# Optimization experiments

Hardware: AMD Instinct MI355X
Metric: run time of the kernel (lower is better)

The kernel has to match this reference:

```python
import jax, jax.numpy as jnp
import numpy as np

# dims matching init_kwargs / input_specs
B, C, H = 8, 256, 48          # input (B, C, H, H)
GRID = 3                       # sqrt(num_memory)
NUM_MEM = GRID * GRID          # 9
WS = H // GRID                 # window_size = 16
S = 128                        # num_slots
D = WS * WS * C                # slot_dim = 65536
K = 5                          # gumbel top-k threshold (shrink_thres, int)
EPS = 1e-12


def setup_inputs() -> dict:
    key = jax.random.key(0)
    k1, k2, k3 = jax.random.split(key, 3)
    stdv = 1.0 / np.sqrt(D)
    x = jax.random.normal(k1, (B, C, H, H), dtype=jnp.float32)
    mem1 = jax.random.uniform(k2, (NUM_MEM, S, D), jnp.float32, -stdv, stdv)
    mem2 = jax.random.uniform(k3, (NUM_MEM, S, D), jnp.float32, -stdv, stdv)
    return {"x": x, "mem1": mem1, "mem2": mem2}


def _window_partition(x):
    # (B, C, H, W) -> (B, NUM_MEM, WS*WS*C); per-window layout is (ws, ws, C) row-major,
    # matching torch unfold -> view(B,C,ws^2,L) -> permute(0,3,2,1).
    b = x.shape[0]
    x = jnp.transpose(x, (0, 2, 3, 1))                        # (B, H, W, C)
    x = x.reshape(b, GRID, WS, GRID, WS, C)
    x = jnp.transpose(x, (0, 1, 3, 2, 4, 5))                  # (B, gh, gw, ws, ws, C)
    return x.reshape(b, NUM_MEM, WS * WS * C)


def _window_reverse(w):
    # (B, NUM_MEM, WS*WS*C) -> (B, C, H, W); exact inverse of _window_partition.
    b = w.shape[0]
    w = w.reshape(b, GRID, GRID, WS, WS, C)
    w = jnp.transpose(w, (0, 1, 3, 2, 4, 5)).reshape(b, H, H, C)
    return jnp.transpose(w, (0, 3, 1, 2))


def _hard_shrink_relu(y, lambd):
    d = y - lambd
    return jax.nn.relu(d) * y / (jnp.abs(d) + EPS)


def _memory_read(q, mem):
    # q: (B, M, D) window queries; mem: (M, S, D) per-window memory matrices.
    att = jnp.einsum('bmd,msd->bms', q, mem)                  # (B, M, S)
    y = jax.nn.softmax(att, axis=-1)
    k = min(S - 1, K)
    thres = jax.lax.top_k(y, k)[0][..., -1:]                  # kth largest per row
    y_hard = _hard_shrink_relu(y, thres)
    y_hard = y_hard / jnp.maximum(jnp.sum(jnp.abs(y_hard), axis=-1, keepdims=True), EPS)
    y_hard = jax.lax.stop_gradient(y_hard - y) + y            # straight-through
    return jnp.einsum('bms,msd->bmd', y_hard, mem)            # (B, M, D)


def reference(x, mem1, mem2):
    # CRU modeled as identity split: x1 = x2 = x (CRU source not provided).
    q = _window_partition(x)                                  # (B, 9, D)
    out1 = _window_reverse(_memory_read(q, mem1))
    out2 = _window_reverse(_memory_read(q, mem2))
    return out1 + out2                                        # eval mode: no bernoulli mask
```

## Files before the change

### kernel.cpp

```cpp
#include <hip/hip_runtime.h>
#include <hip/hip_bf16.h>
#include <cstdint>

#define Bn 8
#define Cn 256
#define Hn 48
#define NUM_MEM 9
#define WSZ 16
#define Sn 128
#define Dn 65536
#define KTOP 5
#define ND2 16

__global__ __launch_bounds__(256) void k_x2q(const float* __restrict__ x,
                                             float* __restrict__ q) {
    const int h = blockIdx.x;
    const int b = blockIdx.y;
    const int gh = h >> 4, i = h & 15;
    __shared__ float tile[Cn * Hn];
    const float* xp = x + (size_t)b * Cn * Hn * Hn + (size_t)h * Hn;
    for (int o = threadIdx.x; o < Cn * Hn; o += blockDim.x) {
        int c = o / Hn, w = o - c * Hn;
        tile[o] = xp[(size_t)c * Hn * Hn + w];
    }
    __syncthreads();
    for (int gw = 0; gw < 3; ++gw) {
        float* qp = q + (size_t)(b * NUM_MEM + gh * 3 + gw) * Dn + i * (WSZ * Cn);
        for (int l = threadIdx.x; l < WSZ * Cn; l += blockDim.x) {
            int j = l >> 8, c = l & 255;
            qp[l] = tile[c * Hn + gw * WSZ + j];
        }
    }
}

__global__ __launch_bounds__(256) void k_att3(const float* __restrict__ q,
                                              const float* __restrict__ mem1,
                                              const float* __restrict__ mem2,
                                              float* __restrict__ ap) {
    const int dseg = blockIdx.x;
    const int mw   = blockIdx.y;
    const int sgrp = blockIdx.z;
    const int e    = sgrp >> 3;
    const int lane = threadIdx.x & 63, wave = threadIdx.x >> 6;
    const int s0   = (sgrp & 7) * 16 + wave * 4;

    const float4* mem4 = (const float4*)(e ? mem2 : mem1);
    const float4* q4   = (const float4*)q;

    const int off0 = dseg * 1024 + lane;
    const float4* mr[4];
    const float4* qr[8];
#pragma unroll
    for (int r = 0; r < 4; ++r)
        mr[r] = mem4 + (size_t)(mw * Sn + s0 + r) * (Dn / 4) + off0;
#pragma unroll
    for (int b = 0; b < 8; ++b)
        qr[b] = q4 + (size_t)(b * NUM_MEM + mw) * (Dn / 4) + off0;

    float a[32];
#pragma unroll
    for (int i = 0; i < 32; ++i) a[i] = 0.f;

    float4 M[4], Q[8];
#pragma unroll
    for (int r = 0; r < 4; ++r) M[r] = mr[r][0];
#pragma unroll
    for (int b = 0; b < 8; ++b) Q[b] = qr[b][0];

    for (int step = 0; step < 16; ++step) {
        const int noff = (step < 15 ? step + 1 : step) * 64;
        float4 Mn[4], Qn[8];
#pragma unroll
        for (int r = 0; r < 4; ++r) Mn[r] = mr[r][noff];
#pragma unroll
        for (int b = 0; b < 8; ++b) Qn[b] = qr[b][noff];

#pragma unroll
        for (int r = 0; r < 4; ++r)
#pragma unroll
            for (int b = 0; b < 8; ++b) {
                a[r * 8 + b] += M[r].x * Q[b].x + M[r].y * Q[b].y
                              + M[r].z * Q[b].z + M[r].w * Q[b].w;
            }
#pragma unroll
        for (int r = 0; r < 4; ++r) M[r] = Mn[r];
#pragma unroll
        for (int b = 0; b < 8; ++b) Q[b] = Qn[b];
    }

#pragma unroll
    for (int k = 0; k < 5; ++k) {
        const int mk = 1 << k;
        const bool up = (lane & mk) != 0;
#pragma unroll
        for (int j = 0; j < (32 >> (k + 1)); ++j) {
            float lo = a[2 * j], hi = a[2 * j + 1];
            float mine = up ? hi : lo;
            float oth  = __shfl_xor(up ? lo : hi, mk, 64);
            a[j] = mine + oth;
        }
    }
    float rsum = a[0] + __shfl_xor(a[0], 32, 64);
    if (lane < 32) {
        const int b = lane & 7, r = (lane >> 3) & 3;
        const int s = s0 + r;
        ap[((size_t)dseg * 144 + (size_t)(e * 8 + b) * 9 + mw) * Sn + s] = rsum;
    }
}

__global__ __launch_bounds__(128) void k_smax(const float* __restrict__ ap,
                                              float* __restrict__ w) {
    const int row = blockIdx.x;
    const int t = threadIdx.x;
    __shared__ float sf[Sn];
    __shared__ unsigned long long sk[Sn];

    float v = 0.f;
#pragma unroll
    for (int nd = 0; nd < ND2; ++nd)
        v += ap[((size_t)nd * 144 + row) * Sn + t];

    sf[t] = v; __syncthreads();
    for (int s = 64; s > 0; s >>= 1) { if (t < s) sf[t] = fmaxf(sf[t], sf[t + s]); __syncthreads(); }
    float mx = sf[0]; __syncthreads();

    float e = expf(v - mx);
    sf[t] = e; __syncthreads();
    for (int s = 64; s > 0; s >>= 1) { if (t < s) sf[t] += sf[t + s]; __syncthreads(); }
    float sum = sf[0]; __syncthreads();
    float y = e / sum;

    bool alive = true;
    float thres = 0.f;
    unsigned int ybits = __float_as_uint(y);
    for (int it = 0; it < KTOP; ++it) {
        sk[t] = alive ? ((((unsigned long long)ybits) << 32) | (unsigned)t) : 0ull;
        __syncthreads();
        for (int s = 64; s > 0; s >>= 1) {
            if (t < s) { if (sk[t + s] > sk[t]) sk[t] = sk[t + s]; }
            __syncthreads();
        }
        unsigned long long kmax = sk[0];
        __syncthreads();
        if ((unsigned)(kmax & 0xffffffffull) == (unsigned)t) alive = false;
        thres = __uint_as_float((unsigned)(kmax >> 32));
    }

    float d   = y - thres;
    float num = fmaxf(d, 0.f) * y;
    float yh  = num / (fabsf(d) + 1e-12f);

    sf[t] = yh; __syncthreads();
    for (int s = 64; s > 0; s >>= 1) { if (t < s) sf[t] += sf[t + s]; __syncthreads(); }
    float l1 = sf[0];
    w[(size_t)row * Sn + t] = yh / fmaxf(l1, 1e-12f);
}

__global__ __launch_bounds__(256) void k_acc(const float* __restrict__ w,
                                             const float* __restrict__ mem1,
                                             const float* __restrict__ mem2,
                                             float* __restrict__ acc) {
    const int chunk = blockIdx.x;
    const int m     = blockIdx.y;
    const int b     = blockIdx.z;
    __shared__ int   nz[2];
    __shared__ int   idx[2][16];
    __shared__ float wv[2][16];
    if (threadIdx.x < 2) nz[threadIdx.x] = 0;
    __syncthreads();
    {
        int eidx = threadIdx.x >> 7;
        int s    = threadIdx.x & 127;
        float ww = w[((size_t)(eidx * Bn + b) * NUM_MEM + m) * Sn + s];
        if (ww != 0.f) {
            int p = atomicAdd(&nz[eidx], 1);
            if (p < 16) { idx[eidx][p] = s; wv[eidx][p] = ww; }
        }
    }
    __syncthreads();
    const int n1 = nz[0], n2 = nz[1];
    const size_t mbase = (size_t)m * Sn * Dn;
    const int dbase = chunk * 4096;
    for (int l = threadIdx.x * 4; l < 4096; l += 1024) {
        int d = dbase + l;
        float4 a = {0.f, 0.f, 0.f, 0.f};
        for (int j = 0; j < n1; ++j) {
            const float4 r = *(const float4*)(mem1 + mbase + (size_t)idx[0][j] * Dn + d);
            float ww = wv[0][j];
            a.x += ww * r.x; a.y += ww * r.y; a.z += ww * r.z; a.w += ww * r.w;
        }
        for (int j = 0; j < n2; ++j) {
            const float4 r = *(const float4*)(mem2 + mbase + (size_t)idx[1][j] * Dn + d);
            float ww = wv[1][j];
            a.x += ww * r.x; a.y += ww * r.y; a.z += ww * r.z; a.w += ww * r.w;
        }
        *(float4*)(acc + (size_t)(b * NUM_MEM + m) * Dn + d) = a;
    }
}

__global__ __launch_bounds__(256) void k_q2x(const float* __restrict__ acc,
                                             float* __restrict__ out) {
    const int h = blockIdx.x;
    const int b = blockIdx.y;
    const int gh = h >> 4, i = h & 15;
    __shared__ float tile[Cn * Hn];
    for (int gw = 0; gw < 3; ++gw) {
        const float* ap = acc + (size_t)(b * NUM_MEM + gh * 3 + gw) * Dn + i * (WSZ * Cn);
        for (int l = threadIdx.x; l < WSZ * Cn; l += blockDim.x) {
            int j = l >> 8, c = l & 255;
            tile[c * Hn + gw * WSZ + j] = ap[l];
        }
    }
    __syncthreads();
    float* op = out + (size_t)b * Cn * Hn * Hn + (size_t)h * Hn;
    for (int o = threadIdx.x; o < Cn * Hn; o += blockDim.x) {
        int c = o / Hn, wcol = o - c * Hn;
        op[(size_t)c * Hn * Hn + wcol] = tile[o];
    }
}

extern "C" void kernel_launch(void* const* d_in, const int* in_sizes, int n_in,
                              void* d_out, int out_size, void* d_ws, size_t ws_size,
                              hipStream_t stream) {
    const float* x    = (const float*)d_in[0];
    const float* mem1 = (const float*)d_in[1];
    const float* mem2 = (const float*)d_in[2];
    float* out = (float*)d_out;

    float* q    = (float*)d_ws;
    float* wbuf = q + (size_t)Bn * NUM_MEM * Dn;
    float* ap   = (float*)d_out;

    k_x2q<<<dim3(Hn, Bn), 256, 0, stream>>>(x, q);
    k_att3<<<dim3(ND2, NUM_MEM, 16), 256, 0, stream>>>(q, mem1, mem2, ap);
    k_smax<<<2 * Bn * NUM_MEM, 128, 0, stream>>>(ap, wbuf);
    k_acc<<<dim3(16, NUM_MEM, Bn), 256, 0, stream>>>(wbuf, mem1, mem2, q );
    k_q2x<<<dim3(Hn, Bn), 256, 0, stream>>>(q, out);
}
```

Baseline: 233.7 us.

## Split attention dot products into finer D chunks for more blocks

The attention kernel now splits D into 128 chunks instead of 16. Each block loads two float4s per lane per memory row up front, with no software-pipelined loop, and processes the batch queries in two halves to limit register pressure. This gives eight times as many blocks, which should raise occupancy and memory-level parallelism on the bandwidth-bound 600MB memory read. The cost is a larger partial-sum buffer that the softmax kernel must reduce over 128 partials instead of 16.

```diff
diff --git a/kernel.cpp b/kernel.cpp
--- a/kernel.cpp
+++ b/kernel.cpp
@@ -10,7 +10,7 @@
 #define Sn 128
 #define Dn 65536
 #define KTOP 5
-#define ND2 16
+#define NDC 128
 
 __global__ __launch_bounds__(256) void k_x2q(const float* __restrict__ x,
                                              float* __restrict__ q) {
@@ -33,59 +33,52 @@
     }
 }
 
-__global__ __launch_bounds__(256) void k_att3(const float* __restrict__ q,
+__global__ __launch_bounds__(256) void k_att4(const float* __restrict__ q,
                                               const float* __restrict__ mem1,
                                               const float* __restrict__ mem2,
                                               float* __restrict__ ap) {
-    const int dseg = blockIdx.x;
-    const int mw   = blockIdx.y;
-    const int sgrp = blockIdx.z;
-    const int e    = sgrp >> 3;
+    const int dc = blockIdx.x;
+    const int mw = blockIdx.y;
+    const int sg = blockIdx.z;
+    const int e  = sg >> 3;
     const int lane = threadIdx.x & 63, wave = threadIdx.x >> 6;
-    const int s0   = (sgrp & 7) * 16 + wave * 4;
+    const int s0 = (sg & 7) * 16 + wave * 4;
 
     const float4* mem4 = (const float4*)(e ? mem2 : mem1);
     const float4* q4   = (const float4*)q;
-
-    const int off0 = dseg * 1024 + lane;
-    const float4* mr[4];
-    const float4* qr[8];
-#pragma unroll
-    for (int r = 0; r < 4; ++r)
-        mr[r] = mem4 + (size_t)(mw * Sn + s0 + r) * (Dn / 4) + off0;
-#pragma unroll
-    for (int b = 0; b < 8; ++b)
-        qr[b] = q4 + (size_t)(b * NUM_MEM + mw) * (Dn / 4) + off0;
+    const int off = dc * 128 + lane;
+
+    float4 M[4][2];
+#pragma unroll
+    for (int r = 0; r < 4; ++r) {
+        const float4* mp = mem4 + (size_t)(mw * Sn + s0 + r) * (Dn / 4) + off;
+        M[r][0] = mp[0];
+        M[r][1] = mp[64];
+    }
 
     float a[32];
 #pragma unroll
     for (int i = 0; i < 32; ++i) a[i] = 0.f;
 
-    float4 M[4], Q[8];
-#pragma unroll
-    for (int r = 0; r < 4; ++r) M[r] = mr[r][0];
-#pragma unroll
-    for (int b = 0; b < 8; ++b) Q[b] = qr[b][0];
-
-    for (int step = 0; step < 16; ++step) {
-        const int noff = (step < 15 ? step + 1 : step) * 64;
-        float4 Mn[4], Qn[8];
-#pragma unroll
-        for (int r = 0; r < 4; ++r) Mn[r] = mr[r][noff];
-#pragma unroll
-        for (int b = 0; b < 8; ++b) Qn[b] = qr[b][noff];
-
+#pragma unroll
+    for (int half = 0; half < 2; ++half) {
+        float4 Q[4][2];
+#pragma unroll
+        for (int b = 0; b < 4; ++b) {
+            const float4* qp = q4 + (size_t)((half * 4 + b) * NUM_MEM + mw) * (Dn / 4) + off;
+            Q[b][0] = qp[0];
+            Q[b][1] = qp[64];
+        }
 #pragma unroll
         for (int r = 0; r < 4; ++r)
 #pragma unroll
-            for (int b = 0; b < 8; ++b) {
-                a[r * 8 + b] += M[r].x * Q[b].x + M[r].y * Q[b].y
-                              + M[r].z * Q[b].z + M[r].w * Q[b].w;
+            for (int b = 0; b < 4; ++b) {
+                const int bi = half * 4 + b;
+                a[r * 8 + bi] += M[r][0].x * Q[b][0].x + M[r][0].y * Q[b][0].y
+                               + M[r][0].z * Q[b][0].z + M[r][0].w * Q[b][0].w
+                               + M[r][1].x * Q[b][1].x + M[r][1].y * Q[b][1].y
+                               + M[r][1].z * Q[b][1].z + M[r][1].w * Q[b][1].w;
             }
-#pragma unroll
-        for (int r = 0; r < 4; ++r) M[r] = Mn[r];
-#pragma unroll
-        for (int b = 0; b < 8; ++b) Q[b] = Qn[b];
     }
 
 #pragma unroll
@@ -103,8 +96,7 @@
     float rsum = a[0] + __shfl_xor(a[0], 32, 64);
     if (lane < 32) {
         const int b = lane & 7, r = (lane >> 3) & 3;
-        const int s = s0 + r;
-        ap[((size_t)dseg * 144 + (size_t)(e * 8 + b) * 9 + mw) * Sn + s] = rsum;
+        ap[((size_t)dc * 144 + (size_t)(e * 8 + b) * 9 + mw) * Sn + (s0 + r)] = rsum;
     }
 }
 
@@ -116,8 +108,8 @@
     __shared__ unsigned long long sk[Sn];
 
     float v = 0.f;
-#pragma unroll
-    for (int nd = 0; nd < ND2; ++nd)
+#pragma unroll 8
+    for (int nd = 0; nd < NDC; ++nd)
         v += ap[((size_t)nd * 144 + row) * Sn + t];
 
     sf[t] = v; __syncthreads();
@@ -232,7 +224,7 @@
     float* ap   = (float*)d_out;
 
     k_x2q<<<dim3(Hn, Bn), 256, 0, stream>>>(x, q);
-    k_att3<<<dim3(ND2, NUM_MEM, 16), 256, 0, stream>>>(q, mem1, mem2, ap);
+    k_att4<<<dim3(NDC, NUM_MEM, 16), 256, 0, stream>>>(q, mem1, mem2, ap);
     k_smax<<<2 * Bn * NUM_MEM, 128, 0, stream>>>(ap, wbuf);
     k_acc<<<dim3(16, NUM_MEM, Bn), 256, 0, stream>>>(wbuf, mem1, mem2, q );
     k_q2x<<<dim3(Hn, Bn), 256, 0, stream>>>(q, out);
```

Measured after the change: 224.5 us. 3.9% less time.
